# Kernel optimization log

Hardware: AMD Instinct MI355X
Metric: run time of the kernel (lower is better)

Reference implementation:

```python
import jax, jax.numpy as jnp
import numpy as np

B, G, IN, H, OUT = 4096, 8, 512, 1024, 64


def setup_inputs() -> dict:
    key = jax.random.key(0)
    k0, k1, k2, k3 = jax.random.split(key, 4)
    x = jax.random.normal(k0, (B, IN), dtype=jnp.float32)
    gid = jax.random.randint(k1, (B,), 0, G, dtype=jnp.int32)
    # Per-group 2-layer MLP params (Kaiming-ish scaling)
    W1 = jax.random.normal(k2, (G, IN, H), dtype=jnp.float32) / np.sqrt(IN)
    b1 = jnp.zeros((G, H), dtype=jnp.float32)
    W2 = jax.random.normal(k3, (G, H, OUT), dtype=jnp.float32) / np.sqrt(H)
    b2 = jnp.zeros((G, OUT), dtype=jnp.float32)
    return {"x": x, "gid": gid, "W1": W1, "b1": b1, "W2": W2, "b2": b2}


def reference(x, gid, W1, b1, W2, b2):
    # Routed 2-layer MLP: each sample i uses expert head gid[i].
    # Compute all G group GEMMs (grouped-GEMM style), then select the
    # routed row per sample with a one-hot contraction (no [B,IN,H]
    # per-sample weight materialization).
    onehot = jax.nn.one_hot(gid, W1.shape[0], dtype=x.dtype)  # [B, G]
    h_all = jnp.einsum('bi,gih->bgh', x, W1) + b1[None]       # [B, G, H]
    h = jax.nn.relu(jnp.einsum('bgh,bg->bh', h_all, onehot))  # [B, H]
    y_all = jnp.einsum('bh,gho->bgo', h, W2) + b2[None]       # [B, G, OUT]
    y = jnp.einsum('bgo,bg->bo', y_all, onehot)               # [B, OUT]
    return y
```

## Files before the change

kernel.cpp:

```cpp
#include <hip/hip_runtime.h>
#include <hip/hip_bf16.h>

#define B_ 4096
#define G_ 8
#define IN_ 512
#define H_ 1024
#define OUT_ 64
#define MAXT64 72
#define MAXT32 136

typedef float f32x4 __attribute__((ext_vector_type(4)));
typedef __bf16 bf16x8 __attribute__((ext_vector_type(8)));
typedef unsigned short u16x8 __attribute__((ext_vector_type(8)));

__device__ inline unsigned short f2bf(float f) {
  unsigned int u = __builtin_bit_cast(unsigned int, f);
  u += 0x7fffu + ((u >> 16) & 1u);
  return (unsigned short)(u >> 16);
}

__device__ inline u16x8 pack8(float4 a, float4 b) {
  return u16x8{f2bf(a.x), f2bf(a.y), f2bf(a.z), f2bf(a.w),
               f2bf(b.x), f2bf(b.y), f2bf(b.z), f2bf(b.w)};
}

__device__ inline void gload16(const void* g, void* l) {
  __builtin_amdgcn_global_load_lds(
      (const __attribute__((address_space(1))) void*)(unsigned long long)g,
      (__attribute__((address_space(3))) void*)(unsigned int)(unsigned long long)l,
      16, 0, 0);
}

__device__ inline bool tile_lookup(const int* __restrict__ meta, int mt,
                                   int shift, int& g, int& row0, int& start,
                                   int& cnt) {
  int ts = 0;
  bool found = false;
#pragma unroll
  for (int gg = 0; gg < G_; gg++) {
    int s = meta[gg], e = meta[gg + 1];
    int T = (e - s + (1 << shift) - 1) >> shift;
    if (!found && mt >= ts && mt < ts + T) {
      g = gg;
      row0 = (mt - ts) << shift;
      start = s;
      cnt = e - s;
      found = true;
    }
    ts += T;
  }
  return found;
}

__global__ __launch_bounds__(256) void prep_kernel(
    const float* __restrict__ W1, const float* __restrict__ W2,
    const float* __restrict__ x, const int* __restrict__ gid,
    unsigned short* __restrict__ W1t, unsigned short* __restrict__ W2t,
    unsigned short* __restrict__ xb, int* __restrict__ meta,
    int* __restrict__ perm) {
  int b = blockIdx.x;
  int t = threadIdx.x;
  if (b < 4096) {
    __shared__ float tile[32][33];
    int h32 = b & 31, k32 = (b >> 5) & 15, g = b >> 9;
    int kl = t >> 3, nl = (t & 7) * 4;
    const float* src =
        W1 + ((size_t)g * IN_ + k32 * 32 + kl) * H_ + h32 * 32 + nl;
    float4 v = *(const float4*)src;
    tile[kl][nl + 0] = v.x;
    tile[kl][nl + 1] = v.y;
    tile[kl][nl + 2] = v.z;
    tile[kl][nl + 3] = v.w;
    __syncthreads();
    int nl2 = t >> 3, kl2 = (t & 7) * 4;
    ushort4 o;
    o.x = f2bf(tile[kl2 + 0][nl2]);
    o.y = f2bf(tile[kl2 + 1][nl2]);
    o.z = f2bf(tile[kl2 + 2][nl2]);
    o.w = f2bf(tile[kl2 + 3][nl2]);
    *(ushort4*)(W1t + ((size_t)g * H_ + h32 * 32 + nl2) * IN_ + k32 * 32 +
                kl2) = o;
  } else if (b < 4608) {
    __shared__ float tile2[32][33];
    int bb = b - 4096;
    int g = bb >> 6, k32 = (bb >> 1) & 31, n32 = bb & 1;
    int kl = t >> 3, nl = (t & 7) * 4;
    const float* src =
        W2 + ((size_t)g * H_ + k32 * 32 + kl) * OUT_ + n32 * 32 + nl;
    float4 v = *(const float4*)src;
    tile2[kl][nl + 0] = v.x;
    tile2[kl][nl + 1] = v.y;
    tile2[kl][nl + 2] = v.z;
    tile2[kl][nl + 3] = v.w;
    __syncthreads();
    int nl2 = t >> 3, kl2 = (t & 7) * 4;
    ushort4 o;
    o.x = f2bf(tile2[kl2 + 0][nl2]);
    o.y = f2bf(tile2[kl2 + 1][nl2]);
    o.z = f2bf(tile2[kl2 + 2][nl2]);
    o.w = f2bf(tile2[kl2 + 3][nl2]);
    *(ushort4*)(W2t + ((size_t)g * OUT_ + n32 * 32 + nl2) * H_ + k32 * 32 +
                kl2) = o;
  } else if (b < 5632) {
    int bb = b - 4608;
    size_t base = (size_t)bb * 2048 + t * 8;
    float4 v0 = *(const float4*)(x + base);
    float4 v1 = *(const float4*)(x + base + 4);
    *(u16x8*)(xb + base) = pack8(v0, v1);
  } else {
    __shared__ unsigned short lc[G_][256];
    __shared__ int offs_s[G_ + 1];
#pragma unroll
    for (int g = 0; g < G_; g++) lc[g][t] = 0;
    int myg[16];
    const int base = t * 16;
    __syncthreads();
#pragma unroll
    for (int j = 0; j < 16; j++) {
      myg[j] = gid[base + j];
      lc[myg[j]][t]++;
    }
    __syncthreads();
    {
      int g = t >> 5, k = t & 31;
      unsigned short pref[8];
      int s = 0;
#pragma unroll
      for (int j = 0; j < 8; j++) {
        pref[j] = (unsigned short)s;
        s += lc[g][8 * k + j];
      }
      int incl = s;
#pragma unroll
      for (int d = 1; d < 32; d <<= 1) {
        int o = __shfl_up(incl, d, 32);
        if (k >= d) incl += o;
      }
      int excl = incl - s;
      if (k == 31) offs_s[g + 1] = incl;
#pragma unroll
      for (int j = 0; j < 8; j++)
        lc[g][8 * k + j] = (unsigned short)(excl + pref[j]);
    }
    __syncthreads();
    if (t == 0) {
      int o = 0;
      for (int g = 0; g < G_; g++) {
        int c = offs_s[g + 1];
        offs_s[g] = o;
        meta[g] = o;
        o += c;
      }
      offs_s[G_] = o;
      meta[G_] = o;
    }
    __syncthreads();
    int cur[G_];
#pragma unroll
    for (int g = 0; g < G_; g++) cur[g] = offs_s[g] + (int)lc[g][t];
#pragma unroll
    for (int j = 0; j < 16; j++) {
      int g = myg[j];
      perm[cur[g]++] = base + j;
    }
  }
}

__global__ __launch_bounds__(256) void gemm1_kernel(
    const unsigned short* __restrict__ xb,
    const unsigned short* __restrict__ W1t, const float* __restrict__ b1,
    const int* __restrict__ meta, const int* __restrict__ perm,
    unsigned short* __restrict__ hb) {
  int b = blockIdx.x;
  int mt = b >> 3, nt = b & 7;
  int g, row0, start, cnt;
  if (!tile_lookup(meta, mt, 6, g, row0, start, cnt)) return;
  int n0 = nt * 128;

  __shared__ __attribute__((aligned(16))) unsigned short As[2][64 * 64];
  __shared__ __attribute__((aligned(16))) unsigned short Bs[2][128 * 64];
  __shared__ int rows[64];

  int tid = threadIdx.x;
  int lane = tid & 63;
  int wv = tid >> 6;

  if (tid < 64) rows[tid] = perm[start + min(row0 + tid, cnt - 1)];
  __syncthreads();

  const unsigned short* asrc[2];
#pragma unroll
  for (int j = 0; j < 2; j++) {
    int pp = j * 2048 + tid * 8;
    int r = pp >> 6;
    int cpos = (pp >> 3) & 7;
    asrc[j] = xb + (size_t)rows[r] * IN_ + ((cpos ^ (r & 7)) << 3);
  }
  const unsigned short* bsrc[4];
#pragma unroll
  for (int j = 0; j < 4; j++) {
    int pp = j * 2048 + tid * 8;
    int r = pp >> 6;
    int cpos = (pp >> 3) & 7;
    bsrc[j] = W1t + ((size_t)g * H_ + n0 + r) * IN_ + ((cpos ^ (r & 7)) << 3);
  }

  int fl = lane & 15, q = lane >> 4;
  int wm0 = (wv >> 1) * 32, wn0 = (wv & 1) * 64;

  f32x4 acc[2][4];
#pragma unroll
  for (int i = 0; i < 2; i++)
#pragma unroll
    for (int j = 0; j < 4; j++) acc[i][j] = f32x4{0.f, 0.f, 0.f, 0.f};

  auto stage = [&](int buf, int k0) {
#pragma unroll
    for (int j = 0; j < 2; j++)
      gload16(asrc[j] + k0, &As[buf][j * 2048 + wv * 512]);
#pragma unroll
    for (int j = 0; j < 4; j++)
      gload16(bsrc[j] + k0, &Bs[buf][j * 2048 + wv * 512]);
  };

  stage(0, 0);
  __syncthreads();

  for (int it = 0; it < 8; it++) {
    int p = it & 1;
    if (it < 7) stage(p ^ 1, (it + 1) * 64);
#pragma unroll
    for (int s = 0; s < 2; s++) {
      int off = (((s << 2) + q) ^ (fl & 7)) << 3;
      bf16x8 a0 = *(const bf16x8*)&As[p][(wm0 + fl) * 64 + off];
      bf16x8 a1 = *(const bf16x8*)&As[p][(wm0 + 16 + fl) * 64 + off];
      bf16x8 b0 = *(const bf16x8*)&Bs[p][(wn0 + fl) * 64 + off];
      bf16x8 b1v = *(const bf16x8*)&Bs[p][(wn0 + 16 + fl) * 64 + off];
      bf16x8 b2v = *(const bf16x8*)&Bs[p][(wn0 + 32 + fl) * 64 + off];
      bf16x8 b3v = *(const bf16x8*)&Bs[p][(wn0 + 48 + fl) * 64 + off];
      acc[0][0] = __builtin_amdgcn_mfma_f32_16x16x32_bf16(a0, b0, acc[0][0], 0, 0, 0);
      acc[0][1] = __builtin_amdgcn_mfma_f32_16x16x32_bf16(a0, b1v, acc[0][1], 0, 0, 0);
      acc[0][2] = __builtin_amdgcn_mfma_f32_16x16x32_bf16(a0, b2v, acc[0][2], 0, 0, 0);
      acc[0][3] = __builtin_amdgcn_mfma_f32_16x16x32_bf16(a0, b3v, acc[0][3], 0, 0, 0);
      acc[1][0] = __builtin_amdgcn_mfma_f32_16x16x32_bf16(a1, b0, acc[1][0], 0, 0, 0);
      acc[1][1] = __builtin_amdgcn_mfma_f32_16x16x32_bf16(a1, b1v, acc[1][1], 0, 0, 0);
      acc[1][2] = __builtin_amdgcn_mfma_f32_16x16x32_bf16(a1, b2v, acc[1][2], 0, 0, 0);
      acc[1][3] = __builtin_amdgcn_mfma_f32_16x16x32_bf16(a1, b3v, acc[1][3], 0, 0, 0);
    }
    __syncthreads();
  }

#pragma unroll
  for (int ni = 0; ni < 4; ni++) {
    int col = n0 + wn0 + ni * 16 + fl;
    float bias = b1[g * H_ + col];
#pragma unroll
    for (int mi = 0; mi < 2; mi++) {
#pragma unroll
      for (int rg = 0; rg < 4; rg++) {
        int rl = wm0 + mi * 16 + q * 4 + rg;
        if (row0 + rl < cnt) {
          float v = fmaxf(acc[mi][ni][rg] + bias, 0.f);
          hb[(size_t)(start + row0 + rl) * H_ + col] = f2bf(v);
        }
      }
    }
  }
}

__global__ __launch_bounds__(256) void gemm2_kernel(
    const unsigned short* __restrict__ hb,
    const unsigned short* __restrict__ W2t, const float* __restrict__ b2,
    const int* __restrict__ meta, const int* __restrict__ perm,
    float* __restrict__ y) {
  int mt = blockIdx.x;
  int g, row0, start, cnt;
  if (!tile_lookup(meta, mt, 5, g, row0, start, cnt)) return;

  __shared__ __attribute__((aligned(16))) unsigned short As2[2][32 * 128];
  __shared__ __attribute__((aligned(16))) unsigned short Bs2[2][64 * 128];
  __shared__ int rows[32];

  int tid = threadIdx.x;
  int lane = tid & 63;
  int wv = tid >> 6;

  if (tid < 32) rows[tid] = perm[start + min(row0 + tid, cnt - 1)];

  const unsigned short* asrc[2];
#pragma unroll
  for (int j = 0; j < 2; j++) {
    int pp = j * 2048 + tid * 8;
    int r = pp >> 7;
    int cpos = (pp >> 3) & 15;
    asrc[j] = hb + (size_t)(start + min(row0 + r, cnt - 1)) * H_ +
              ((cpos ^ (r & 7)) << 3);
  }
  const unsigned short* bsrc[4];
#pragma unroll
  for (int j = 0; j < 4; j++) {
    int pp = j * 2048 + tid * 8;
    int r = pp >> 7;
    int cpos = (pp >> 3) & 15;
    bsrc[j] = W2t + ((size_t)g * OUT_ + r) * H_ + ((cpos ^ (r & 7)) << 3);
  }

  int fl = lane & 15, q = lane >> 4;
  int wm0 = (wv >> 1) * 16, wn0 = (wv & 1) * 32;

  f32x4 acc[2];
  acc[0] = f32x4{0.f, 0.f, 0.f, 0.f};
  acc[1] = f32x4{0.f, 0.f, 0.f, 0.f};

  auto stage = [&](int buf, int k0) {
#pragma unroll
    for (int j = 0; j < 2; j++)
      gload16(asrc[j] + k0, &As2[buf][j * 2048 + wv * 512]);
#pragma unroll
    for (int j = 0; j < 4; j++)
      gload16(bsrc[j] + k0, &Bs2[buf][j * 2048 + wv * 512]);
  };

  stage(0, 0);
  __syncthreads();

  for (int it = 0; it < 8; it++) {
    int p = it & 1;
    if (it < 7) stage(p ^ 1, (it + 1) * 128);
#pragma unroll
    for (int s = 0; s < 4; s++) {
      int off = (((s << 2) + q) ^ (fl & 7)) << 3;
      bf16x8 a0 = *(const bf16x8*)&As2[p][(wm0 + fl) * 128 + off];
      bf16x8 b0 = *(const bf16x8*)&Bs2[p][(wn0 + fl) * 128 + off];
      bf16x8 b1v = *(const bf16x8*)&Bs2[p][(wn0 + 16 + fl) * 128 + off];
      acc[0] = __builtin_amdgcn_mfma_f32_16x16x32_bf16(a0, b0, acc[0], 0, 0, 0);
      acc[1] = __builtin_amdgcn_mfma_f32_16x16x32_bf16(a0, b1v, acc[1], 0, 0, 0);
    }
    __syncthreads();
  }

#pragma unroll
  for (int ni = 0; ni < 2; ni++) {
    int col = wn0 + ni * 16 + fl;
    float bias = b2[g * OUT_ + col];
#pragma unroll
    for (int rg = 0; rg < 4; rg++) {
      int rl = wm0 + q * 4 + rg;
      if (row0 + rl < cnt) {
        y[(size_t)rows[rl] * OUT_ + col] = acc[ni][rg] + bias;
      }
    }
  }
}

extern "C" void kernel_launch(void* const* d_in, const int* in_sizes, int n_in,
                              void* d_out, int out_size, void* d_ws,
                              size_t ws_size, hipStream_t stream) {
  const float* x = (const float*)d_in[0];
  const int* gid = (const int*)d_in[1];
  const float* W1 = (const float*)d_in[2];
  const float* b1 = (const float*)d_in[3];
  const float* W2 = (const float*)d_in[4];
  const float* b2 = (const float*)d_in[5];
  float* y = (float*)d_out;

  int* meta = (int*)d_ws;
  int* perm = (int*)((char*)d_ws + 64);
  unsigned short* W1t = (unsigned short*)((char*)d_ws + (1u << 16));
  unsigned short* W2t = (unsigned short*)((char*)d_ws + (16u << 20));
  unsigned short* xb = (unsigned short*)((char*)d_ws + (24u << 20));
  unsigned short* hb = (unsigned short*)((char*)d_ws + (32u << 20));

  prep_kernel<<<5633, 256, 0, stream>>>(W1, W2, x, gid, W1t, W2t, xb, meta,
                                        perm);
  gemm1_kernel<<<MAXT64 * 8, 256, 0, stream>>>(xb, W1t, b1, meta, perm, hb);
  gemm2_kernel<<<MAXT32, 256, 0, stream>>>(hb, W2t, b2, meta, perm, y);
}
```

Baseline: 105.8 us.

## Triple-buffer LDS staging with vmcnt-gated barriers in both grouped GEMMs

Both GEMM kernels move from double-buffered LDS staging with a full __syncthreads per iteration to three buffers. Each iteration waits only for the oldest outstanding global_load_lds batch (s_waitcnt vmcnt) before the barrier, so two tiles can be in flight during compute. gemm1 also drops the shared rows table and its barrier, reading the permutation index straight into the source addresses. The cost is more LDS per block (72KB in gemm1), which may lower how many blocks fit on a CU, and the vmcnt counts rely on each stage issuing exactly six loads.

```diff
diff --git a/kernel.cpp b/kernel.cpp
--- a/kernel.cpp
+++ b/kernel.cpp
@@ -30,6 +30,13 @@
       (__attribute__((address_space(3))) void*)(unsigned int)(unsigned long long)l,
       16, 0, 0);
 }
+
+#define WAITED_BARRIER(VM)                                   \
+  {                                                          \
+    asm volatile("s_waitcnt vmcnt(" #VM ")" ::: "memory");   \
+    __builtin_amdgcn_sched_barrier(0);                       \
+    __builtin_amdgcn_s_barrier();                            \
+  }
 
 __device__ inline bool tile_lookup(const int* __restrict__ meta, int mt,
                                    int shift, int& g, int& row0, int& start,
@@ -177,16 +184,12 @@
   if (!tile_lookup(meta, mt, 6, g, row0, start, cnt)) return;
   int n0 = nt * 128;
 
-  __shared__ __attribute__((aligned(16))) unsigned short As[2][64 * 64];
-  __shared__ __attribute__((aligned(16))) unsigned short Bs[2][128 * 64];
-  __shared__ int rows[64];
+  __shared__ __attribute__((aligned(16))) unsigned short As[3][64 * 64];
+  __shared__ __attribute__((aligned(16))) unsigned short Bs[3][128 * 64];
 
   int tid = threadIdx.x;
   int lane = tid & 63;
   int wv = tid >> 6;
-
-  if (tid < 64) rows[tid] = perm[start + min(row0 + tid, cnt - 1)];
-  __syncthreads();
 
   const unsigned short* asrc[2];
 #pragma unroll
@@ -194,7 +197,8 @@
     int pp = j * 2048 + tid * 8;
     int r = pp >> 6;
     int cpos = (pp >> 3) & 7;
-    asrc[j] = xb + (size_t)rows[r] * IN_ + ((cpos ^ (r & 7)) << 3);
+    int prow = perm[start + min(row0 + r, cnt - 1)];
+    asrc[j] = xb + (size_t)prow * IN_ + ((cpos ^ (r & 7)) << 3);
   }
   const unsigned short* bsrc[4];
 #pragma unroll
@@ -223,12 +227,7 @@
       gload16(bsrc[j] + k0, &Bs[buf][j * 2048 + wv * 512]);
   };
 
-  stage(0, 0);
-  __syncthreads();
-
-  for (int it = 0; it < 8; it++) {
-    int p = it & 1;
-    if (it < 7) stage(p ^ 1, (it + 1) * 64);
+  auto compute = [&](int p) {
 #pragma unroll
     for (int s = 0; s < 2; s++) {
       int off = (((s << 2) + q) ^ (fl & 7)) << 3;
@@ -247,8 +246,23 @@
       acc[1][2] = __builtin_amdgcn_mfma_f32_16x16x32_bf16(a1, b2v, acc[1][2], 0, 0, 0);
       acc[1][3] = __builtin_amdgcn_mfma_f32_16x16x32_bf16(a1, b3v, acc[1][3], 0, 0, 0);
     }
-    __syncthreads();
-  }
+  };
+
+  stage(0, 0);
+  stage(1, 64);
+#define G1_ITER(T, VM)                              \
+  WAITED_BARRIER(VM);                               \
+  if ((T) + 2 < 8) stage(((T) + 2) % 3, ((T) + 2) * 64); \
+  compute((T) % 3);
+  G1_ITER(0, 6)
+  G1_ITER(1, 6)
+  G1_ITER(2, 6)
+  G1_ITER(3, 6)
+  G1_ITER(4, 6)
+  G1_ITER(5, 6)
+  G1_ITER(6, 6)
+  G1_ITER(7, 0)
+#undef G1_ITER
 
 #pragma unroll
   for (int ni = 0; ni < 4; ni++) {
@@ -277,8 +291,8 @@
   int g, row0, start, cnt;
   if (!tile_lookup(meta, mt, 5, g, row0, start, cnt)) return;
 
-  __shared__ __attribute__((aligned(16))) unsigned short As2[2][32 * 128];
-  __shared__ __attribute__((aligned(16))) unsigned short Bs2[2][64 * 128];
+  __shared__ __attribute__((aligned(16))) unsigned short As2[3][32 * 128];
+  __shared__ __attribute__((aligned(16))) unsigned short Bs2[3][64 * 128];
   __shared__ int rows[32];
 
   int tid = threadIdx.x;
@@ -321,12 +335,7 @@
       gload16(bsrc[j] + k0, &Bs2[buf][j * 2048 + wv * 512]);
   };
 
-  stage(0, 0);
-  __syncthreads();
-
-  for (int it = 0; it < 8; it++) {
-    int p = it & 1;
-    if (it < 7) stage(p ^ 1, (it + 1) * 128);
+  auto compute = [&](int p) {
 #pragma unroll
     for (int s = 0; s < 4; s++) {
       int off = (((s << 2) + q) ^ (fl & 7)) << 3;
@@ -336,8 +345,23 @@
       acc[0] = __builtin_amdgcn_mfma_f32_16x16x32_bf16(a0, b0, acc[0], 0, 0, 0);
       acc[1] = __builtin_amdgcn_mfma_f32_16x16x32_bf16(a0, b1v, acc[1], 0, 0, 0);
     }
-    __syncthreads();
-  }
+  };
+
+  stage(0, 0);
+  stage(1, 128);
+#define G2_ITER(T, VM)                               \
+  WAITED_BARRIER(VM);                                \
+  if ((T) + 2 < 8) stage(((T) + 2) % 3, ((T) + 2) * 128); \
+  compute((T) % 3);
+  G2_ITER(0, 6)
+  G2_ITER(1, 6)
+  G2_ITER(2, 6)
+  G2_ITER(3, 6)
+  G2_ITER(4, 6)
+  G2_ITER(5, 6)
+  G2_ITER(6, 6)
+  G2_ITER(7, 0)
+#undef G2_ITER
 
 #pragma unroll
   for (int ni = 0; ni < 2; ni++) {
```

Measured after the change: 107.2 us. About the same (+1.4%).
